# Performance work log

Hardware: AMD Instinct MI355X
Metric: run time of the kernel (lower is better)

Reference implementation:

```python
import jax, jax.numpy as jnp
import numpy as np

N_Q = 8
DIM = 128
CODEBOOK_SIZE = 1024


def setup_inputs() -> dict:
    key = jax.random.key(0)
    k1, k2 = jax.random.split(key)
    x = jax.random.normal(k1, (8, DIM, 4096), dtype=jnp.float32)
    codebooks = jax.random.normal(k2, (N_Q, CODEBOOK_SIZE, DIM), dtype=jnp.float32)
    return {"x": x, "codebooks": codebooks, "frame_rate": 75}


def _rvq(xt, codebooks):
    # xt: (B, T, D); codebooks: (n_q, K, D)
    def stage(carry, cb):
        residual, qout = carry
        # squared euclidean distance (B, T, K); argmin == Encodec's argmax of -dist
        d = (jnp.sum(residual * residual, axis=-1, keepdims=True)
             - 2.0 * jnp.einsum('btd,kd->btk', residual, cb)
             + jnp.sum(cb * cb, axis=-1))
        idx = jnp.argmin(d, axis=-1)                     # (B, T)
        q = cb[idx]                                       # gather: (B, T, D)
        # commit loss: mse(quantize.detach(), input)
        commit = jnp.mean((jax.lax.stop_gradient(q) - residual) ** 2)
        # straight-through estimator
        q_st = residual + jax.lax.stop_gradient(q - residual)
        return (residual - q_st, qout + q_st), (idx, commit)

    init = (xt, jnp.zeros_like(xt))
    (_, qout), (codes, commits) = jax.lax.scan(stage, init, codebooks)
    return qout, codes, commits


def reference(x, codebooks, frame_rate):
    # x: (B, D, T) -> (B, T, D)
    xt = jnp.swapaxes(x, 1, 2)
    qout, codes, commits = _rvq(xt, codebooks)
    quantized = jnp.swapaxes(qout, 1, 2)                 # (B, D, T)
    n_q, K, _ = codebooks.shape
    bw_per_q = np.log2(K) * frame_rate
    bw = jnp.asarray(n_q * bw_per_q, dtype=jnp.float32)
    penalty = jnp.mean(commits)
    return quantized, codes, bw, penalty
```

## Files before the change

kernel.cpp:

```cpp
#include <hip/hip_runtime.h>
#include <math.h>

#define Bsz 8
#define Dd  128
#define Tt  4096
#define Kk  1024
#define NQ  8
#define BT  (Bsz*Tt)
#define MT  128
#define NTHR 512
#define WV  8

typedef float f32x4 __attribute__((ext_vector_type(4)));
typedef short short8 __attribute__((ext_vector_type(8)));

__device__ __forceinline__ unsigned short f2bf(float x) {
    unsigned u = __float_as_uint(x);
    u += 0x7FFF + ((u >> 16) & 1);
    return (unsigned short)(u >> 16);
}
__device__ __forceinline__ float bf2f(unsigned short h) {
    return __uint_as_float(((unsigned)h) << 16);
}

__device__ __forceinline__ void gload_lds16(const void* g, void* l) {
    __builtin_amdgcn_global_load_lds(
        (const __attribute__((address_space(1))) unsigned int*)g,
        (__attribute__((address_space(3))) unsigned int*)l, 16, 0, 0);
}

__global__ void k_init(const float* __restrict__ x,
                       float* __restrict__ resid) {
    __shared__ float tile[32][33];
    int b  = blockIdx.z;
    int t0 = blockIdx.x * 32, d0 = blockIdx.y * 32;
    int tx = threadIdx.x, ty = threadIdx.y;
    #pragma unroll
    for (int k = 0; k < 4; k++) {
        int d = d0 + ty + k * 8;
        tile[ty + k * 8][tx] = x[((size_t)(b * Dd + d)) * Tt + t0 + tx];
    }
    __syncthreads();
    #pragma unroll
    for (int k = 0; k < 4; k++) {
        int t = t0 + ty + k * 8;
        resid[((size_t)(b * Tt + t)) * Dd + d0 + tx] = tile[tx][ty + k * 8];
    }
}

__global__ void k_prep(const float* __restrict__ cb, char* __restrict__ bswz) {
    int ln = threadIdx.x;
    int kc = blockIdx.x & 3;
    int t  = (blockIdx.x >> 2) & 63;
    int q  = blockIdx.x >> 8;
    int code = t * 16 + (ln & 15);
    int d0   = kc * 32 + (ln >> 4) * 8;
    const float* src = cb + ((size_t)(q * Kk + code)) * Dd + d0;
    float v[8];
    *(float4*)&v[0] = *(const float4*)src;
    *(float4*)&v[4] = *(const float4*)(src + 4);
    short8 h, l;
    #pragma unroll
    for (int j = 0; j < 8; j++) {
        unsigned short hu = f2bf(v[j]);
        h[j] = (short)hu;
        l[j] = (short)f2bf(v[j] - bf2f(hu));
    }
    char* base = bswz + ((size_t)(q * 64 + t)) * 8192;
    *(short8*)(base + kc * 1024 + ln * 16) = h;
    *(short8*)(base + 4096 + kc * 1024 + ln * 16) = l;
}

__global__ void k_c2(const float* __restrict__ cb,
                     float* __restrict__ c2,
                     double* __restrict__ commits) {
    int row  = blockIdx.x * 4 + (threadIdx.x >> 6);
    int lane = threadIdx.x & 63;
    const float* p = cb + (size_t)row * Dd;
    float a = p[lane], b = p[lane + 64];
    float s = a * a + b * b;
    #pragma unroll
    for (int off = 32; off; off >>= 1) s += __shfl_down(s, off);
    if (lane == 0) c2[row] = s;
    if (blockIdx.x == 0 && threadIdx.x < NQ) commits[threadIdx.x] = 0.0;
}

__device__ __forceinline__ float exact_score_sw(const float* __restrict__ rldsb,
                                                int p,
                                                const float* __restrict__ crow,
                                                float c2v) {
    const f32x4* r4 = (const f32x4*)rldsb;
    const f32x4* c4 = (const f32x4*)crow;
    int rb = p * 32, sw = p & 7;
    float a = 0.0f;
    #pragma unroll
    for (int d4 = 0; d4 < 32; d4++) {
        f32x4 r = r4[rb + (d4 ^ sw)];
        f32x4 c = c4[d4];
        a = fmaf(r[0], c[0], a); a = fmaf(r[1], c[1], a);
        a = fmaf(r[2], c[2], a); a = fmaf(r[3], c[3], a);
    }
    return fmaf(-2.0f, a, c2v);
}

__global__ __launch_bounds__(NTHR, 2) void k_rvq_fused(
        float* __restrict__ resid,
        const float* __restrict__ cb,
        const char*  __restrict__ bswz,
        const float* __restrict__ c2g,
        float* __restrict__ codes_f,
        double* __restrict__ commits) {
    __shared__ float rlds[MT * Dd];
    __shared__ float c2s[Kk];
    __shared__ f32x4 bbuf[2][4][512];
    __shared__ float winp[MT];
    __shared__ float wmax[WV];
    __shared__ float fb1[MT], fb2[MT], fb3[MT];
    __shared__ int   sidxs[MT];
    __shared__ int   nfall, flist[MT];
    __shared__ float csum[WV];

    const int tid  = threadIdx.x;
    const int w    = tid >> 6, ln = tid & 63;
    const int quad = ln >> 4,  m  = ln & 15;
    const int base = blockIdx.x * MT;
    const int prow = w * 16 + m;

    f32x4* r4 = (f32x4*)rlds;

    {
        const f32x4* src = (const f32x4*)(resid + (size_t)base * Dd);
        #pragma unroll
        for (int i = 0; i < (MT * Dd / 4) / NTHR; i++) {
            int idx = tid + i * NTHR;
            int row = idx >> 5, c4 = idx & 31;
            r4[row * 32 + (c4 ^ (row & 7))] = src[idx];
        }
    }
    {
        const char* srcb = bswz + (size_t)w * 1024 + (size_t)ln * 16;
        char* dstb = (char*)&bbuf[0][0][0] + w * 1024;
        #pragma unroll
        for (int t = 0; t < 4; t++)
            gload_lds16(srcb + t * 8192, dstb + t * 8192);
    }
    int par = 0;
    asm volatile("s_waitcnt vmcnt(0)" ::: "memory");
    __syncthreads();

    #pragma unroll 1
    for (int q = 0; q < NQ; q++) {
        const float* cbq = cb + (size_t)q * Kk * Dd;
        c2s[tid]        = c2g[q * Kk + tid];
        c2s[tid + NTHR] = c2g[q * Kk + tid + NTHR];
        if (tid == 0) nfall = 0;
        __syncthreads();

        float lm = fmaxf(c2s[tid], c2s[tid + NTHR]);
        #pragma unroll
        for (int off = 32; off; off >>= 1) lm = fmaxf(lm, __shfl_xor(lm, off));
        if (ln == 0) wmax[w] = lm;
        __syncthreads();
        float cm2 = wmax[0];
        #pragma unroll
        for (int w2 = 1; w2 < WV; w2++) cm2 = fmaxf(cm2, wmax[w2]);
        float cmaxq = sqrtf(cm2);

        short8 Ah[4], Al[4];
        float r2p = 0.0f;
        #pragma unroll
        for (int kc = 0; kc < 4; kc++) {
            int c4a = kc * 8 + quad * 2;
            float v[8];
            *(f32x4*)&v[0] = r4[prow * 32 + (c4a ^ (prow & 7))];
            *(f32x4*)&v[4] = r4[prow * 32 + ((c4a + 1) ^ (prow & 7))];
            short8 h, l;
            #pragma unroll
            for (int j = 0; j < 8; j++) {
                unsigned short hu = f2bf(v[j]);
                h[j] = (short)hu;
                l[j] = (short)f2bf(v[j] - bf2f(hu));
                r2p  = fmaf(v[j], v[j], r2p);
            }
            Ah[kc] = h; Al[kc] = l;
        }
        r2p += __shfl_xor(r2p, 16);
        r2p += __shfl_xor(r2p, 32);
        {
            float R  = sqrtf(r2p);
            float sb = fmaf(2.0f * R, cmaxq, cmaxq * cmaxq);
            float p2 = exp2f(ceilf(log2f(fmaxf(sb, 2.0f))));
            if (quad == 0) winp[prow] = 0.05f + p2 * (1.0f / 4096.0f);
        }

        float b1[4], b2[4], b3[4];
        #pragma unroll
        for (int j = 0; j < 4; j++) {
            b1[j] = INFINITY; b2[j] = INFINITY; b3[j] = INFINITY;
        }
        __syncthreads();

        #pragma unroll 1
        for (int jq = 0; jq < 16; jq++) {
            const int g = q * 16 + jq;
            if (g + 1 < NQ * 16) {
                const char* srcb = bswz + (size_t)(g + 1) * 32768
                                 + (size_t)w * 1024 + (size_t)ln * 16;
                char* dstb = (char*)&bbuf[par ^ 1][0][0] + w * 1024;
                #pragma unroll
                for (int t = 0; t < 4; t++)
                    gload_lds16(srcb + t * 8192, dstb + t * 8192);
            }
            #pragma unroll
            for (int t = 0; t < 4; t++) {
                const short8* Bt = (const short8*)&bbuf[par][t][0];
                f32x4 a01 = {0.f, 0.f, 0.f, 0.f};
                f32x4 a23 = {0.f, 0.f, 0.f, 0.f};
                #pragma unroll
                for (int kc = 0; kc < 4; kc++) {
                    short8 ch = Bt[kc * 64 + ln];
                    short8 cl = Bt[256 + kc * 64 + ln];
                    if (kc < 2) {
                        a01 = __builtin_amdgcn_mfma_f32_16x16x32_bf16(Al[kc], ch, a01, 0, 0, 0);
                        a01 = __builtin_amdgcn_mfma_f32_16x16x32_bf16(Ah[kc], cl, a01, 0, 0, 0);
                        a01 = __builtin_amdgcn_mfma_f32_16x16x32_bf16(Ah[kc], ch, a01, 0, 0, 0);
                    } else {
                        a23 = __builtin_amdgcn_mfma_f32_16x16x32_bf16(Al[kc], ch, a23, 0, 0, 0);
                        a23 = __builtin_amdgcn_mfma_f32_16x16x32_bf16(Ah[kc], cl, a23, 0, 0, 0);
                        a23 = __builtin_amdgcn_mfma_f32_16x16x32_bf16(Ah[kc], ch, a23, 0, 0, 0);
                    }
                }
                const int codei = (4 * jq + t) * 16 + m;
                const float c2v = c2s[codei];
                const unsigned codeu = (unsigned)codei;
                #pragma unroll
                for (int j = 0; j < 4; j++) {
                    float s = fmaf(-2.0f, a01[j] + a23[j], c2v);
                    float sp = __uint_as_float(
                        (__float_as_uint(s) & 0xFFFFFC00u) | codeu);
                    b3[j] = __builtin_amdgcn_fmed3f(sp, b2[j], b3[j]);
                    b2[j] = __builtin_amdgcn_fmed3f(sp, b1[j], b2[j]);
                    b1[j] = fminf(b1[j], sp);
                }
            }
            asm volatile("s_waitcnt vmcnt(0)" ::: "memory");
            __syncthreads();
            par ^= 1;
        }

        #pragma unroll
        for (int j = 0; j < 4; j++) {
            float v1 = b1[j], v2 = b2[j], v3 = b3[j];
            #pragma unroll
            for (int off = 1; off < 16; off <<= 1) {
                float w1 = __shfl_xor(v1, off);
                float w2 = __shfl_xor(v2, off);
                float w3 = __shfl_xor(v3, off);
                bool aw = v1 < w1;
                float x2 = aw ? v2 : w2, x3 = aw ? v3 : w3;
                float z1 = aw ? w1 : v1, z2 = aw ? w2 : v2;
                v1 = fminf(v1, w1);
                bool s2 = x2 < z1;
                v2 = fminf(x2, z1);
                v3 = s2 ? fminf(x3, z1) : fminf(x2, z2);
            }
            if (m == 0) {
                int p = w * 16 + quad * 4 + j;
                fb1[p] = v1; fb2[p] = v2; fb3[p] = v3;
            }
        }
        __syncthreads();

        if (tid < MT) {
            int p = tid;
            float v1 = fb1[p], v2 = fb2[p], v3 = fb3[p];
            int   a1 = (int)(__float_as_uint(v1) & 1023u);
            int   a2 = (int)(__float_as_uint(v2) & 1023u);
            float win = winp[p];
            if (v3 <= v1 + win) {
                int sl = atomicAdd(&nfall, 1);
                flist[sl] = p;
            } else {
                int bk = a1;
                if (v2 <= v1 + win) {
                    float s1 = exact_score_sw(rlds, p, cbq + (size_t)a1 * Dd, c2s[a1]);
                    float s2e = exact_score_sw(rlds, p, cbq + (size_t)a2 * Dd, c2s[a2]);
                    if (s2e < s1 || (s2e == s1 && a2 < a1)) bk = a2;
                }
                sidxs[p] = bk;
                codes_f[(size_t)q * BT + base + p] = (float)bk;
            }
        }
        __syncthreads();

        {
            int nf = nfall;
            for (int fi0 = 0; fi0 < nf; fi0 += WV) {
                int fi = fi0 + w;
                if (fi < nf) {
                    int p = flist[fi];
                    float bv = INFINITY; int bk = 0;
                    #pragma unroll 4
                    for (int c = 0; c < 16; c++) {
                        int k = c * 64 + ln;
                        float sc = exact_score_sw(rlds, p,
                                                  cbq + (size_t)k * Dd, c2s[k]);
                        if (sc < bv || (sc == bv && k < bk)) { bv = sc; bk = k; }
                    }
                    #pragma unroll
                    for (int off = 32; off; off >>= 1) {
                        float v2 = __shfl_xor(bv, off);
                        int   k2 = __shfl_xor(bk, off);
                        if (v2 < bv || (v2 == bv && k2 < bk)) { bv = v2; bk = k2; }
                    }
                    if (ln == 0) {
                        sidxs[p] = bk;
                        codes_f[(size_t)q * BT + base + p] = (float)bk;
                    }
                }
            }
        }
        __syncthreads();

        {
            int p = tid >> 2;
            int rb = p * 32, sw = p & 7, cb4 = (tid & 3) * 8;
            const float* qrow = cbq + ((size_t)sidxs[p]) * Dd + (tid & 3) * 32;
            float cacc = 0.0f;
            #pragma unroll
            for (int hh = 0; hh < 8; hh++) {
                f32x4 r  = r4[rb + ((cb4 + hh) ^ sw)];
                f32x4 qv = *(const f32x4*)(qrow + hh * 4);
                float t1x = qv[0] - r[0], t1y = qv[1] - r[1];
                float t1z = qv[2] - r[2], t1w = qv[3] - r[3];
                float qsx = r[0] + t1x, qsy = r[1] + t1y;
                float qsz = r[2] + t1z, qsw = r[3] + t1w;
                f32x4 nr = { r[0] - qsx, r[1] - qsy, r[2] - qsz, r[3] - qsw };
                r4[rb + ((cb4 + hh) ^ sw)] = nr;
                cacc = fmaf(t1x, t1x, cacc); cacc = fmaf(t1y, t1y, cacc);
                cacc = fmaf(t1z, t1z, cacc); cacc = fmaf(t1w, t1w, cacc);
            }
            #pragma unroll
            for (int off = 32; off; off >>= 1) cacc += __shfl_down(cacc, off);
            if (ln == 0) csum[w] = cacc;
        }
        __syncthreads();
        if (tid == 0) {
            double sd = 0.0;
            #pragma unroll
            for (int w2 = 0; w2 < WV; w2++) sd += (double)csum[w2];
            atomicAdd(commits + q, sd);
        }
        __syncthreads();
    }

    {
        f32x4* dst = (f32x4*)(resid + (size_t)base * Dd);
        #pragma unroll
        for (int i = 0; i < (MT * Dd / 4) / NTHR; i++) {
            int idx = tid + i * NTHR;
            int row = idx >> 5, c4 = idx & 31;
            dst[idx] = r4[row * 32 + (c4 ^ (row & 7))];
        }
    }
}

__global__ void k_final(const float* __restrict__ x,
                        const float* __restrict__ resid,
                        float* __restrict__ outq) {
    __shared__ float tile[32][33];
    int b  = blockIdx.z;
    int t0 = blockIdx.x * 32, d0 = blockIdx.y * 32;
    int tx = threadIdx.x, ty = threadIdx.y;
    #pragma unroll
    for (int k = 0; k < 4; k++) {
        int t = t0 + ty + k * 8;
        tile[ty + k * 8][tx] = resid[((size_t)(b * Tt + t)) * Dd + d0 + tx];
    }
    __syncthreads();
    #pragma unroll
    for (int k = 0; k < 4; k++) {
        int d = d0 + ty + k * 8;
        size_t o = ((size_t)(b * Dd + d)) * Tt + t0 + tx;
        outq[o] = x[o] - tile[tx][ty + k * 8];
    }
}

__global__ void k_scalars(const double* __restrict__ commits,
                          const int* __restrict__ frame_rate,
                          float* __restrict__ outs) {
    if (threadIdx.x == 0 && blockIdx.x == 0) {
        double s = 0.0;
        #pragma unroll
        for (int q = 0; q < NQ; q++) s += commits[q];
        double per_elem = s / ((double)NQ * (double)BT * (double)Dd);
        outs[0] = (float)(NQ * 10.0 * (double)frame_rate[0]);
        outs[1] = (float)per_elem;
    }
}

extern "C" void kernel_launch(void* const* d_in, const int* in_sizes, int n_in,
                              void* d_out, int out_size, void* d_ws, size_t ws_size,
                              hipStream_t stream) {
    const float* x  = (const float*)d_in[0];
    const float* cb = (const float*)d_in[1];
    const int*   fr = (const int*)d_in[2];

    float* outq    = (float*)d_out;
    float* codes_f = outq + (size_t)Bsz * Dd * Tt;
    float* scal    = codes_f + (size_t)NQ * BT;

    char* ws = (char*)d_ws;
    float*    resid   = (float*)ws;
    float*    c2      = resid + (size_t)BT * Dd;
    double*   commits = (double*)(c2 + (size_t)NQ * Kk);
    size_t    off     = (size_t)((char*)(commits + NQ) - ws);
    char*     bswz    = ws + ((off + 255) & ~(size_t)255);

    dim3 tb(32, 8, 1);
    k_init<<<dim3(Tt / 32, Dd / 32, Bsz), tb, 0, stream>>>(x, resid);
    k_prep<<<NQ * 256, 64, 0, stream>>>(cb, bswz);
    k_c2<<<NQ * Kk / 4, 256, 0, stream>>>(cb, c2, commits);

    k_rvq_fused<<<BT / MT, NTHR, 0, stream>>>(resid, cb, bswz, c2,
                                              codes_f, commits);

    k_final<<<dim3(Tt / 32, Dd / 32, Bsz), tb, 0, stream>>>(x, resid, outq);
    k_scalars<<<1, 64, 0, stream>>>(commits, fr, scal);
}
```

Baseline: 469.1 us.

## Fuse input transpose and output subtraction into the RVQ kernel

```diff
diff --git a/kernel.cpp b/kernel.cpp
--- a/kernel.cpp
+++ b/kernel.cpp
@@ -27,25 +27,6 @@
     __builtin_amdgcn_global_load_lds(
         (const __attribute__((address_space(1))) unsigned int*)g,
         (__attribute__((address_space(3))) unsigned int*)l, 16, 0, 0);
-}
-
-__global__ void k_init(const float* __restrict__ x,
-                       float* __restrict__ resid) {
-    __shared__ float tile[32][33];
-    int b  = blockIdx.z;
-    int t0 = blockIdx.x * 32, d0 = blockIdx.y * 32;
-    int tx = threadIdx.x, ty = threadIdx.y;
-    #pragma unroll
-    for (int k = 0; k < 4; k++) {
-        int d = d0 + ty + k * 8;
-        tile[ty + k * 8][tx] = x[((size_t)(b * Dd + d)) * Tt + t0 + tx];
-    }
-    __syncthreads();
-    #pragma unroll
-    for (int k = 0; k < 4; k++) {
-        int t = t0 + ty + k * 8;
-        resid[((size_t)(b * Tt + t)) * Dd + d0 + tx] = tile[tx][ty + k * 8];
-    }
 }
 
 __global__ void k_prep(const float* __restrict__ cb, char* __restrict__ bswz) {
@@ -104,12 +85,13 @@
 }
 
 __global__ __launch_bounds__(NTHR, 2) void k_rvq_fused(
-        float* __restrict__ resid,
+        const float* __restrict__ x,
         const float* __restrict__ cb,
         const char*  __restrict__ bswz,
         const float* __restrict__ c2g,
         float* __restrict__ codes_f,
-        double* __restrict__ commits) {
+        double* __restrict__ commits,
+        float* __restrict__ outq) {
     __shared__ float rlds[MT * Dd];
     __shared__ float c2s[Kk];
     __shared__ f32x4 bbuf[2][4][512];
@@ -124,17 +106,21 @@
     const int w    = tid >> 6, ln = tid & 63;
     const int quad = ln >> 4,  m  = ln & 15;
     const int base = blockIdx.x * MT;
+    const int b    = base >> 12;
+    const int t0   = base & (Tt - 1);
     const int prow = w * 16 + m;
 
     f32x4* r4 = (f32x4*)rlds;
 
     {
-        const f32x4* src = (const f32x4*)(resid + (size_t)base * Dd);
-        #pragma unroll
-        for (int i = 0; i < (MT * Dd / 4) / NTHR; i++) {
-            int idx = tid + i * NTHR;
-            int row = idx >> 5, c4 = idx & 31;
-            r4[row * 32 + (c4 ^ (row & 7))] = src[idx];
+        const int i  = tid >> 2;
+        const int dc = tid & 3;
+        const float* xb = x + ((size_t)b * Dd) * Tt + t0 + i;
+        #pragma unroll
+        for (int d4 = 0; d4 < 32; d4++) {
+            int d = d4 * 4 + dc;
+            float v = xb[(size_t)d * Tt];
+            rlds[i * 128 + ((d4 ^ (i & 7)) << 2) + dc] = v;
         }
     }
     {
@@ -355,34 +341,16 @@
     }
 
     {
-        f32x4* dst = (f32x4*)(resid + (size_t)base * Dd);
-        #pragma unroll
-        for (int i = 0; i < (MT * Dd / 4) / NTHR; i++) {
-            int idx = tid + i * NTHR;
-            int row = idx >> 5, c4 = idx & 31;
-            dst[idx] = r4[row * 32 + (c4 ^ (row & 7))];
-        }
-    }
-}
-
-__global__ void k_final(const float* __restrict__ x,
-                        const float* __restrict__ resid,
-                        float* __restrict__ outq) {
-    __shared__ float tile[32][33];
-    int b  = blockIdx.z;
-    int t0 = blockIdx.x * 32, d0 = blockIdx.y * 32;
-    int tx = threadIdx.x, ty = threadIdx.y;
-    #pragma unroll
-    for (int k = 0; k < 4; k++) {
-        int t = t0 + ty + k * 8;
-        tile[ty + k * 8][tx] = resid[((size_t)(b * Tt + t)) * Dd + d0 + tx];
-    }
-    __syncthreads();
-    #pragma unroll
-    for (int k = 0; k < 4; k++) {
-        int d = d0 + ty + k * 8;
-        size_t o = ((size_t)(b * Dd + d)) * Tt + t0 + tx;
-        outq[o] = x[o] - tile[tx][ty + k * 8];
+        const int i  = tid >> 2;
+        const int dc = tid & 3;
+        const size_t xb = ((size_t)b * Dd) * Tt + t0 + i;
+        #pragma unroll
+        for (int d4 = 0; d4 < 32; d4++) {
+            int d = d4 * 4 + dc;
+            size_t o = xb + (size_t)d * Tt;
+            float r = rlds[i * 128 + ((d4 ^ (i & 7)) << 2) + dc];
+            outq[o] = x[o] - r;
+        }
     }
 }
 
@@ -417,14 +385,11 @@
     size_t    off     = (size_t)((char*)(commits + NQ) - ws);
     char*     bswz    = ws + ((off + 255) & ~(size_t)255);
 
-    dim3 tb(32, 8, 1);
-    k_init<<<dim3(Tt / 32, Dd / 32, Bsz), tb, 0, stream>>>(x, resid);
     k_prep<<<NQ * 256, 64, 0, stream>>>(cb, bswz);
     k_c2<<<NQ * Kk / 4, 256, 0, stream>>>(cb, c2, commits);
 
-    k_rvq_fused<<<BT / MT, NTHR, 0, stream>>>(resid, cb, bswz, c2,
-                                              codes_f, commits);
-
-    k_final<<<dim3(Tt / 32, Dd / 32, Bsz), tb, 0, stream>>>(x, resid, outq);
+    k_rvq_fused<<<BT / MT, NTHR, 0, stream>>>(x, cb, bswz, c2,
+                                              codes_f, commits, outq);
+
     k_scalars<<<1, 64, 0, stream>>>(commits, fr, scal);
 }
```

Result: no change. 473.5 us (+0.9%).
